# Kernel tuning notes

Hardware: AMD Instinct MI355X
Metric: run time of the kernel (lower is better)

The kernel has to match this reference:

```python
import jax, jax.numpy as jnp
import numpy as np

N_NODES = 100000
N_EDGES = 1600000
D_IN = 128
D_OUT = 128
EPS = 1e-5


def setup_inputs() -> dict:
    key = jax.random.key(0)
    k1, k2, k3, k4, k5 = jax.random.split(key, 5)
    x = jax.random.normal(k1, (N_NODES, D_IN), dtype=jnp.float32)
    row = jax.random.randint(k2, (N_EDGES,), 0, N_NODES, dtype=jnp.int64)
    col = jax.random.randint(k3, (N_EDGES,), 0, N_NODES, dtype=jnp.int64)
    adj_vals = jax.random.uniform(k4, (N_EDGES,), dtype=jnp.float32)
    # Xavier-uniform init for weight, zeros for bias (as in the torch module)
    limit = float(np.sqrt(6.0 / (D_IN + D_OUT)))
    weight = jax.random.uniform(k5, (D_IN, D_OUT), minval=-limit, maxval=limit, dtype=jnp.float32)
    bias = jnp.zeros((D_OUT,), dtype=jnp.float32)
    return {"x": x, "row": row, "col": col, "adj_vals": adj_vals, "weight": weight, "bias": bias}


def reference(x, row, col, adj_vals, weight, bias):
    # degree = row-sum of sparse adj
    degree = jax.ops.segment_sum(adj_vals, row, num_segments=N_NODES)
    degree = jnp.where(degree == 0, EPS, degree)
    d_inv_sqrt = (degree + EPS) ** -0.5  # [N]
    # edge-wise symmetric normalization: D^-1/2 A D^-1/2
    edge_w = d_inv_sqrt[row] * adj_vals * d_inv_sqrt[col]  # [E]
    # SpMM: gather neighbor features, scale, scatter-add to destination rows
    msgs = edge_w[:, None] * x[col]  # [E, D_IN]
    agg = jax.ops.segment_sum(msgs, row, num_segments=N_NODES)  # [N, D_IN]
    return agg @ weight + bias
```

## Files before the change

kernel.cpp:

```cpp
#include <hip/hip_runtime.h>

#define NN 100000
#define NE 1600000
#define D  128
#define EPS 1e-5f

#define NBKT   782
#define NEB    391
#define EPB_H  4096
#define NSCAN  (NBKT*NEB)
#define GRID2  299
#define CAP    2560
#define SLW    16

#define OFF_HCNT 0x0000000ULL
#define OFF_PART 0x0140000ULL
#define OFF_DINV 0x0150000ULL
#define OFF_RBC  0x0200000ULL
#define OFF_GREC 0x0280000ULL
#define OFF_ECOL 0x0F00000ULL
#define OFF_YB   0x1700000ULL

typedef short short8 __attribute__((ext_vector_type(8)));
typedef float f32x4 __attribute__((ext_vector_type(4)));

static __device__ __forceinline__ unsigned f2bf(float f) {
    unsigned u = __float_as_uint(f);
    return (u + 0x7fffu + ((u >> 16) & 1u)) >> 16;
}

__global__ void k0h(const int* __restrict__ row, unsigned* __restrict__ hcnt) {
    __shared__ unsigned h[NBKT];
    int t = threadIdx.x, b = blockIdx.x;
    for (int i = t; i < NBKT; i += 256) h[i] = 0;
    __syncthreads();
    int ebeg = b * EPB_H;
    for (int i = t; i < EPB_H; i += 256) {
        int e = ebeg + i;
        if (e < NE) atomicAdd(&h[((unsigned)row[e]) >> 7], 1u);
    }
    __syncthreads();
    for (int i = t; i < NBKT; i += 256) hcnt[i * NEB + b] = h[i];
}

__global__ void k2a(const unsigned* __restrict__ hcnt, unsigned* __restrict__ part) {
    __shared__ unsigned s[256];
    int t = threadIdx.x;
    int gi = blockIdx.x * 1024 + t * 4;
    unsigned v = 0;
    #pragma unroll
    for (int j = 0; j < 4; ++j) if (gi + j < NSCAN) v += hcnt[gi + j];
    s[t] = v;
    __syncthreads();
    for (int d = 128; d > 0; d >>= 1) {
        if (t < d) s[t] += s[t + d];
        __syncthreads();
    }
    if (t == 0) part[blockIdx.x] = s[0];
}

__global__ void k2c(unsigned* __restrict__ hcnt, const unsigned* __restrict__ part) {
    __shared__ unsigned s[256];
    __shared__ unsigned bbase;
    int t = threadIdx.x, g = blockIdx.x;

    unsigned v = 0;
    for (int i = t; i < g; i += 256) v += part[i];
    s[t] = v;
    __syncthreads();
    for (int d = 128; d > 0; d >>= 1) {
        if (t < d) s[t] += s[t + d];
        __syncthreads();
    }
    if (t == 0) bbase = s[0];
    __syncthreads();
    unsigned base = bbase;
    __syncthreads();

    int gi = g * 1024 + t * 4;
    unsigned w[4], tot = 0;
    #pragma unroll
    for (int j = 0; j < 4; ++j) {
        w[j] = (gi + j < NSCAN) ? hcnt[gi + j] : 0;
        tot += w[j];
    }
    s[t] = tot;
    __syncthreads();
    for (int d = 1; d < 256; d <<= 1) {
        unsigned u = (t >= d) ? s[t - d] : 0;
        __syncthreads();
        s[t] += u;
        __syncthreads();
    }
    unsigned run = base + s[t] - tot;
    #pragma unroll
    for (int j = 0; j < 4; ++j) {
        if (gi + j < NSCAN) { hcnt[gi + j] = run; run += w[j]; }
    }
}

__launch_bounds__(256)
__global__ void k3(const int* __restrict__ row, const int* __restrict__ col,
                   const float* __restrict__ adj, const unsigned* __restrict__ hcnt,
                   unsigned long long* __restrict__ grec) {
    __shared__ unsigned cur[NBKT];
    int t = threadIdx.x, b = blockIdx.x;
    for (int i = t; i < NBKT; i += 256) cur[i] = hcnt[i * NEB + b];
    __syncthreads();
    int ebeg = b * EPB_H;
    for (int i = t; i < EPB_H; i += 256) {
        int e = ebeg + i;
        if (e >= NE) continue;
        unsigned r = (unsigned)row[e];
        unsigned aq = (unsigned)rintf(adj[e] * 32767.0f);
        unsigned lo = (unsigned)col[e] | (aq << 17);
        unsigned dst = atomicAdd(&cur[r >> 7], 1u);
        grec[dst] = (unsigned long long)lo | ((unsigned long long)(r & 127u) << 32);
    }
}

__launch_bounds__(256, 2)
__global__ void k1g(const float* __restrict__ x, const float* __restrict__ w,
                    const unsigned* __restrict__ hcnt,
                    const unsigned long long* __restrict__ grec,
                    float* __restrict__ dinv_g, unsigned* __restrict__ rbcnt_g,
                    unsigned* __restrict__ ecol_g, unsigned short* __restrict__ yb) {
    __shared__ unsigned short sx[128 * 128];
    __shared__ unsigned short sw[128 * 128];
    __shared__ unsigned sdeg[128], scnt[128], srb[128], scur[128];
    __shared__ float sdv[128];
    unsigned* secol = (unsigned*)sx;
    int tid = threadIdx.x;
    int b = blockIdx.x;
    int base = b * 128;

    if (tid < 128) { sdeg[tid] = 0; scnt[tid] = 0; }
    __syncthreads();
    unsigned beg = hcnt[b * NEB];
    unsigned end = (b == NBKT - 1) ? NE : hcnt[(b + 1) * NEB];
    unsigned n = end - beg;
    for (unsigned p = beg + tid; p < end; p += 256) {
        unsigned long long rec = grec[p];
        unsigned rid = (unsigned)(rec >> 32) & 127u;
        atomicAdd(&sdeg[rid], ((unsigned)rec >> 17) & 0x7FFFu);
        atomicAdd(&scnt[rid], 1u);
    }
    __syncthreads();

    if (tid < 128) {
        float d = (float)sdeg[tid] * (1.0f / 32767.0f);
        d = (d == 0.0f) ? EPS : d;
        float dv = rsqrtf(d + EPS);
        sdv[tid] = dv;
        int r = base + tid;
        if (r < NN) dinv_g[r] = dv;
        srb[tid] = scnt[tid];
    }
    __syncthreads();
    for (int dd = 1; dd < 128; dd <<= 1) {
        unsigned u = (tid >= dd && tid < 128) ? srb[tid - dd] : 0;
        __syncthreads();
        if (tid < 128) srb[tid] += u;
        __syncthreads();
    }
    if (tid < 128) {
        unsigned rb = srb[tid] - scnt[tid];
        srb[tid] = rb;
        scur[tid] = rb;
        rbcnt_g[b * 128 + tid] = (rb << 16) | scnt[tid];
    }
    __syncthreads();

    for (unsigned p = beg + tid; p < end; p += 256) {
        unsigned long long rec = grec[p];
        unsigned rank = atomicAdd(&scur[(unsigned)(rec >> 32) & 127u], 1u);
        if (rank < CAP) secol[rank] = (unsigned)rec;
    }
    __syncthreads();
    unsigned ns = min(n, (unsigned)CAP);
    for (unsigned i = tid; i < ns; i += 256) ecol_g[(size_t)b * CAP + i] = secol[i];
    __syncthreads();

    #pragma unroll
    for (int i = 0; i < 8; ++i) {
        int task = i * 256 + tid;
        int nn = task & 127, ko = task >> 7;
        const float* wp = w + (size_t)(ko * 8) * D + nn;
        uint4 pk;
        pk.x = f2bf(wp[0])     | (f2bf(wp[D])     << 16);
        pk.y = f2bf(wp[2 * D]) | (f2bf(wp[3 * D]) << 16);
        pk.z = f2bf(wp[4 * D]) | (f2bf(wp[5 * D]) << 16);
        pk.w = f2bf(wp[6 * D]) | (f2bf(wp[7 * D]) << 16);
        int idx = (nn * 128 + ko * 8) ^ ((nn & 7) << 3);
        *(uint4*)(&sw[idx]) = pk;
    }
    #pragma unroll
    for (int i = 0; i < 8; ++i) {
        int task = i * 256 + tid;
        int ko = task & 15, r = task >> 4;
        int gr = base + r;
        float4 f0 = make_float4(0.f, 0.f, 0.f, 0.f), f1 = f0;
        if (gr < NN) {
            const float* xp = x + (size_t)gr * D + ko * 8;
            f0 = *(const float4*)xp;
            f1 = *(const float4*)(xp + 4);
        }
        uint4 pk;
        pk.x = f2bf(f0.x) | (f2bf(f0.y) << 16);
        pk.y = f2bf(f0.z) | (f2bf(f0.w) << 16);
        pk.z = f2bf(f1.x) | (f2bf(f1.y) << 16);
        pk.w = f2bf(f1.z) | (f2bf(f1.w) << 16);
        int idx = (r * 128 + ko * 8) ^ ((r & 7) << 3);
        *(uint4*)(&sx[idx]) = pk;
    }
    __syncthreads();

    int wv = tid >> 6, l = tid & 63;
    int lr = l & 15, g = l >> 4;

    f32x4 acc[2][8];
    #pragma unroll
    for (int ti = 0; ti < 2; ++ti)
        #pragma unroll
        for (int tj = 0; tj < 8; ++tj)
            acc[ti][tj] = (f32x4){0.f, 0.f, 0.f, 0.f};

    #pragma unroll
    for (int kc = 0; kc < 4; ++kc) {
        int kb = kc * 32 + g * 8;
        short8 a[2], bb[8];
        #pragma unroll
        for (int ti = 0; ti < 2; ++ti) {
            int r0 = wv * 32 + ti * 16 + lr;
            a[ti] = *(const short8*)(&sx[(r0 * 128 + kb) ^ ((r0 & 7) << 3)]);
        }
        #pragma unroll
        for (int tj = 0; tj < 8; ++tj) {
            int n0 = tj * 16 + lr;
            bb[tj] = *(const short8*)(&sw[(n0 * 128 + kb) ^ ((n0 & 7) << 3)]);
        }
        #pragma unroll
        for (int ti = 0; ti < 2; ++ti)
            #pragma unroll
            for (int tj = 0; tj < 8; ++tj)
                acc[ti][tj] = __builtin_amdgcn_mfma_f32_16x16x32_bf16(
                    a[ti], bb[tj], acc[ti][tj], 0, 0, 0);
    }

    #pragma unroll
    for (int ti = 0; ti < 2; ++ti) {
        #pragma unroll
        for (int reg = 0; reg < 4; ++reg) {
            int lrow = wv * 32 + ti * 16 + g * 4 + reg;
            int gr = base + lrow;
            if (gr < NN) {
                float dv = sdv[lrow];
                #pragma unroll
                for (int tj = 0; tj < 8; ++tj)
                    yb[(size_t)tj * (NN * SLW) + (size_t)gr * SLW + lr] =
                        (unsigned short)f2bf(acc[ti][tj][reg] * dv);
            }
        }
    }
}

__launch_bounds__(512, 4)
__global__ void k4b(const unsigned* __restrict__ rbcnt_g, const unsigned* __restrict__ ecol_g,
                    const float* __restrict__ dinv, const unsigned short* __restrict__ ybs,
                    const float* __restrict__ bias, float* __restrict__ out) {
    __shared__ unsigned ecol[CAP + 8];
    __shared__ unsigned rb_l[128], cnt_l[128];
    __shared__ unsigned nsh;
    int t = threadIdx.x, bid = blockIdx.x;
    int s = bid & 7;
    int q = bid >> 3;
    const unsigned short* ys = ybs + (size_t)s * (NN * SLW);

    if (t < 128) {
        unsigned v = rbcnt_g[q * 128 + t];
        rb_l[t] = v >> 16;
        cnt_l[t] = v & 0xFFFFu;
        if (t == 127) nsh = min((v >> 16) + (v & 0xFFFFu), (unsigned)CAP);
    }
    __syncthreads();
    unsigned n = nsh;
    const unsigned* eg = ecol_g + (size_t)q * CAP;
    for (unsigned i = t; i < n; i += 512) ecol[i] = eg[i];
    __syncthreads();

    int grp = t >> 2, lq = t & 3;
    int r = q * 128 + grp;
    if (r >= NN) return;
    unsigned jb = rb_l[grp];
    unsigned jend = min(jb + cnt_l[grp], (unsigned)CAP);

    float a0 = 0.f, a1 = 0.f, a2 = 0.f, a3 = 0.f;

    for (unsigned j = jb; j < jend; j += 8) {
        unsigned ee[8];
        uint2 yq[8];
        float wv[8];
        int cm[8];
        #pragma unroll
        for (int u = 0; u < 8; ++u) ee[u] = ecol[j + u];
        #pragma unroll
        for (int u = 0; u < 8; ++u) cm[u] = min((int)(ee[u] & 0x1FFFFu), NN - 1);
        #pragma unroll
        for (int u = 0; u < 8; ++u)
            yq[u] = *(const uint2*)(ys + (size_t)cm[u] * SLW + lq * 4);
        #pragma unroll
        for (int u = 0; u < 8; ++u)
            wv[u] = (j + u < jend) ? (float)(ee[u] >> 17) : 0.f;
        #pragma unroll
        for (int u = 0; u < 8; ++u) {
            a0 += wv[u] * __uint_as_float(yq[u].x << 16);
            a1 += wv[u] * __uint_as_float(yq[u].x & 0xffff0000u);
            a2 += wv[u] * __uint_as_float(yq[u].y << 16);
            a3 += wv[u] * __uint_as_float(yq[u].y & 0xffff0000u);
        }
    }

    float scale = dinv[r] * (1.0f / 32767.0f);
    float4 bb = *(const float4*)(bias + s * SLW + lq * 4);
    float4 rr = make_float4(a0 * scale + bb.x, a1 * scale + bb.y,
                            a2 * scale + bb.z, a3 * scale + bb.w);
    *(float4*)(out + (size_t)r * D + s * SLW + lq * 4) = rr;
}

extern "C" void kernel_launch(void* const* d_in, const int* in_sizes, int n_in,
                              void* d_out, int out_size, void* d_ws, size_t ws_size,
                              hipStream_t stream) {
    const float* x    = (const float*)d_in[0];
    const int*   row  = (const int*)d_in[1];
    const int*   col  = (const int*)d_in[2];
    const float* adj  = (const float*)d_in[3];
    const float* wgt  = (const float*)d_in[4];
    const float* bias = (const float*)d_in[5];
    float* out = (float*)d_out;
    char*  ws  = (char*)d_ws;

    unsigned* hcnt  = (unsigned*)(ws + OFF_HCNT);
    unsigned* part  = (unsigned*)(ws + OFF_PART);
    float*    dinv  = (float*)(ws + OFF_DINV);
    unsigned* rbcnt = (unsigned*)(ws + OFF_RBC);
    unsigned long long* grec = (unsigned long long*)(ws + OFF_GREC);
    unsigned* ecolg = (unsigned*)(ws + OFF_ECOL);
    unsigned short* yb = (unsigned short*)(ws + OFF_YB);

    k0h<<<NEB, 256, 0, stream>>>(row, hcnt);
    k2a<<<GRID2, 256, 0, stream>>>(hcnt, part);
    k2c<<<GRID2, 256, 0, stream>>>(hcnt, part);
    k3 <<<NEB, 256, 0, stream>>>(row, col, adj, hcnt, grec);
    k1g<<<NBKT, 256, 0, stream>>>(x, wgt, hcnt, grec, dinv, rbcnt, ecolg, yb);
    k4b<<<NBKT * 8, 512, 0, stream>>>(rbcnt, ecolg, dinv, yb, bias, out);
}
```

Measured before the change: 150.0 us.

## Replace global scan with per-bucket scan into fixed-capacity bucket slots; widen SpMM gathers

```diff
diff --git a/kernel.cpp b/kernel.cpp
--- a/kernel.cpp
+++ b/kernel.cpp
@@ -9,17 +9,16 @@
 #define NEB    391
 #define EPB_H  4096
 #define NSCAN  (NBKT*NEB)
-#define GRID2  299
 #define CAP    2560
 #define SLW    16
 
 #define OFF_HCNT 0x0000000ULL
-#define OFF_PART 0x0140000ULL
+#define OFF_BTOT 0x0140000ULL
 #define OFF_DINV 0x0150000ULL
 #define OFF_RBC  0x0200000ULL
 #define OFF_GREC 0x0280000ULL
-#define OFF_ECOL 0x0F00000ULL
-#define OFF_YB   0x1700000ULL
+#define OFF_ECOL 0x11C6000ULL
+#define OFF_YB   0x1A00000ULL
 
 typedef short short8 __attribute__((ext_vector_type(8)));
 typedef float f32x4 __attribute__((ext_vector_type(4)));
@@ -43,48 +42,14 @@
     for (int i = t; i < NBKT; i += 256) hcnt[i * NEB + b] = h[i];
 }
 
-__global__ void k2a(const unsigned* __restrict__ hcnt, unsigned* __restrict__ part) {
+__global__ void k2s(unsigned* __restrict__ hcnt, unsigned* __restrict__ btot) {
     __shared__ unsigned s[256];
-    int t = threadIdx.x;
-    int gi = blockIdx.x * 1024 + t * 4;
-    unsigned v = 0;
-    #pragma unroll
-    for (int j = 0; j < 4; ++j) if (gi + j < NSCAN) v += hcnt[gi + j];
-    s[t] = v;
-    __syncthreads();
-    for (int d = 128; d > 0; d >>= 1) {
-        if (t < d) s[t] += s[t + d];
-        __syncthreads();
-    }
-    if (t == 0) part[blockIdx.x] = s[0];
-}
-
-__global__ void k2c(unsigned* __restrict__ hcnt, const unsigned* __restrict__ part) {
-    __shared__ unsigned s[256];
-    __shared__ unsigned bbase;
-    int t = threadIdx.x, g = blockIdx.x;
-
-    unsigned v = 0;
-    for (int i = t; i < g; i += 256) v += part[i];
-    s[t] = v;
-    __syncthreads();
-    for (int d = 128; d > 0; d >>= 1) {
-        if (t < d) s[t] += s[t + d];
-        __syncthreads();
-    }
-    if (t == 0) bbase = s[0];
-    __syncthreads();
-    unsigned base = bbase;
-    __syncthreads();
-
-    int gi = g * 1024 + t * 4;
-    unsigned w[4], tot = 0;
-    #pragma unroll
-    for (int j = 0; j < 4; ++j) {
-        w[j] = (gi + j < NSCAN) ? hcnt[gi + j] : 0;
-        tot += w[j];
-    }
-    s[t] = tot;
+    int t = threadIdx.x, b = blockIdx.x;
+    unsigned* hp = hcnt + (size_t)b * NEB;
+    unsigned v0 = (2 * t     < NEB) ? hp[2 * t]     : 0;
+    unsigned v1 = (2 * t + 1 < NEB) ? hp[2 * t + 1] : 0;
+    unsigned sum = v0 + v1;
+    s[t] = sum;
     __syncthreads();
     for (int d = 1; d < 256; d <<= 1) {
         unsigned u = (t >= d) ? s[t - d] : 0;
@@ -92,11 +57,10 @@
         s[t] += u;
         __syncthreads();
     }
-    unsigned run = base + s[t] - tot;
-    #pragma unroll
-    for (int j = 0; j < 4; ++j) {
-        if (gi + j < NSCAN) { hcnt[gi + j] = run; run += w[j]; }
-    }
+    unsigned base = s[t] - sum;
+    if (2 * t     < NEB) hp[2 * t]     = base;
+    if (2 * t + 1 < NEB) hp[2 * t + 1] = base + v0;
+    if (t == 255) btot[b] = s[255];
 }
 
 __launch_bounds__(256)
@@ -105,23 +69,26 @@
                    unsigned long long* __restrict__ grec) {
     __shared__ unsigned cur[NBKT];
     int t = threadIdx.x, b = blockIdx.x;
-    for (int i = t; i < NBKT; i += 256) cur[i] = hcnt[i * NEB + b];
+    for (int i = t; i < NBKT; i += 256)
+        cur[i] = (unsigned)i * CAP + hcnt[i * NEB + b];
     __syncthreads();
     int ebeg = b * EPB_H;
     for (int i = t; i < EPB_H; i += 256) {
         int e = ebeg + i;
         if (e >= NE) continue;
         unsigned r = (unsigned)row[e];
+        unsigned bkt = r >> 7;
         unsigned aq = (unsigned)rintf(adj[e] * 32767.0f);
         unsigned lo = (unsigned)col[e] | (aq << 17);
-        unsigned dst = atomicAdd(&cur[r >> 7], 1u);
-        grec[dst] = (unsigned long long)lo | ((unsigned long long)(r & 127u) << 32);
+        unsigned dst = atomicAdd(&cur[bkt], 1u);
+        if (dst < (bkt + 1) * (unsigned)CAP)
+            grec[dst] = (unsigned long long)lo | ((unsigned long long)(r & 127u) << 32);
     }
 }
 
 __launch_bounds__(256, 2)
 __global__ void k1g(const float* __restrict__ x, const float* __restrict__ w,
-                    const unsigned* __restrict__ hcnt,
+                    const unsigned* __restrict__ btot,
                     const unsigned long long* __restrict__ grec,
                     float* __restrict__ dinv_g, unsigned* __restrict__ rbcnt_g,
                     unsigned* __restrict__ ecol_g, unsigned short* __restrict__ yb) {
@@ -136,9 +103,9 @@
 
     if (tid < 128) { sdeg[tid] = 0; scnt[tid] = 0; }
     __syncthreads();
-    unsigned beg = hcnt[b * NEB];
-    unsigned end = (b == NBKT - 1) ? NE : hcnt[(b + 1) * NEB];
-    unsigned n = end - beg;
+    unsigned beg = (unsigned)b * CAP;
+    unsigned n = min(btot[b], (unsigned)CAP);
+    unsigned end = beg + n;
     for (unsigned p = beg + tid; p < end; p += 256) {
         unsigned long long rec = grec[p];
         unsigned rid = (unsigned)(rec >> 32) & 127u;
@@ -177,8 +144,7 @@
         if (rank < CAP) secol[rank] = (unsigned)rec;
     }
     __syncthreads();
-    unsigned ns = min(n, (unsigned)CAP);
-    for (unsigned i = tid; i < ns; i += 256) ecol_g[(size_t)b * CAP + i] = secol[i];
+    for (unsigned i = tid; i < n; i += 256) ecol_g[(size_t)b * CAP + i] = secol[i];
     __syncthreads();
 
     #pragma unroll
@@ -257,14 +223,14 @@
                 float dv = sdv[lrow];
                 #pragma unroll
                 for (int tj = 0; tj < 8; ++tj)
-                    yb[(size_t)tj * (NN * SLW) + (size_t)gr * SLW + lr] =
+                    yb[(size_t)tj * ((size_t)NN * SLW) + (size_t)gr * SLW + lr] =
                         (unsigned short)f2bf(acc[ti][tj][reg] * dv);
             }
         }
     }
 }
 
-__launch_bounds__(512, 4)
+__launch_bounds__(256, 4)
 __global__ void k4b(const unsigned* __restrict__ rbcnt_g, const unsigned* __restrict__ ecol_g,
                     const float* __restrict__ dinv, const unsigned short* __restrict__ ybs,
                     const float* __restrict__ bias, float* __restrict__ out) {
@@ -274,7 +240,7 @@
     int t = threadIdx.x, bid = blockIdx.x;
     int s = bid & 7;
     int q = bid >> 3;
-    const unsigned short* ys = ybs + (size_t)s * (NN * SLW);
+    const unsigned short* ys = ybs + (size_t)s * ((size_t)NN * SLW);
 
     if (t < 128) {
         unsigned v = rbcnt_g[q * 128 + t];
@@ -285,29 +251,32 @@
     __syncthreads();
     unsigned n = nsh;
     const unsigned* eg = ecol_g + (size_t)q * CAP;
-    for (unsigned i = t; i < n; i += 512) ecol[i] = eg[i];
-    __syncthreads();
-
-    int grp = t >> 2, lq = t & 3;
+    for (unsigned i = t; i < n; i += 256) ecol[i] = eg[i];
+    __syncthreads();
+
+    int grp = t >> 1, lq = t & 1;
     int r = q * 128 + grp;
     if (r >= NN) return;
     unsigned jb = rb_l[grp];
     unsigned jend = min(jb + cnt_l[grp], (unsigned)CAP);
 
     float a0 = 0.f, a1 = 0.f, a2 = 0.f, a3 = 0.f;
+    float a4 = 0.f, a5 = 0.f, a6 = 0.f, a7 = 0.f;
 
     for (unsigned j = jb; j < jend; j += 8) {
         unsigned ee[8];
-        uint2 yq[8];
+        uint4 yq[8];
         float wv[8];
         int cm[8];
+        unsigned c0 = ecol[j] & 0x1FFFFu;
         #pragma unroll
         for (int u = 0; u < 8; ++u) ee[u] = ecol[j + u];
         #pragma unroll
-        for (int u = 0; u < 8; ++u) cm[u] = min((int)(ee[u] & 0x1FFFFu), NN - 1);
-        #pragma unroll
         for (int u = 0; u < 8; ++u)
-            yq[u] = *(const uint2*)(ys + (size_t)cm[u] * SLW + lq * 4);
+            cm[u] = (j + u < jend) ? (int)(ee[u] & 0x1FFFFu) : (int)c0;
+        #pragma unroll
+        for (int u = 0; u < 8; ++u)
+            yq[u] = *(const uint4*)(ys + (size_t)cm[u] * SLW + lq * 8);
         #pragma unroll
         for (int u = 0; u < 8; ++u)
             wv[u] = (j + u < jend) ? (float)(ee[u] >> 17) : 0.f;
@@ -317,14 +286,21 @@
             a1 += wv[u] * __uint_as_float(yq[u].x & 0xffff0000u);
             a2 += wv[u] * __uint_as_float(yq[u].y << 16);
             a3 += wv[u] * __uint_as_float(yq[u].y & 0xffff0000u);
+            a4 += wv[u] * __uint_as_float(yq[u].z << 16);
+            a5 += wv[u] * __uint_as_float(yq[u].z & 0xffff0000u);
+            a6 += wv[u] * __uint_as_float(yq[u].w << 16);
+            a7 += wv[u] * __uint_as_float(yq[u].w & 0xffff0000u);
         }
     }
 
     float scale = dinv[r] * (1.0f / 32767.0f);
-    float4 bb = *(const float4*)(bias + s * SLW + lq * 4);
-    float4 rr = make_float4(a0 * scale + bb.x, a1 * scale + bb.y,
-                            a2 * scale + bb.z, a3 * scale + bb.w);
-    *(float4*)(out + (size_t)r * D + s * SLW + lq * 4) = rr;
+    const float4* bp = (const float4*)(bias + s * SLW + lq * 8);
+    float4* op = (float4*)(out + (size_t)r * D + s * SLW + lq * 8);
+    float4 b0 = bp[0], b1 = bp[1];
+    op[0] = make_float4(a0 * scale + b0.x, a1 * scale + b0.y,
+                        a2 * scale + b0.z, a3 * scale + b0.w);
+    op[1] = make_float4(a4 * scale + b1.x, a5 * scale + b1.y,
+                        a6 * scale + b1.z, a7 * scale + b1.w);
 }
 
 extern "C" void kernel_launch(void* const* d_in, const int* in_sizes, int n_in,
@@ -340,7 +316,7 @@
     char*  ws  = (char*)d_ws;
 
     unsigned* hcnt  = (unsigned*)(ws + OFF_HCNT);
-    unsigned* part  = (unsigned*)(ws + OFF_PART);
+    unsigned* btot  = (unsigned*)(ws + OFF_BTOT);
     float*    dinv  = (float*)(ws + OFF_DINV);
     unsigned* rbcnt = (unsigned*)(ws + OFF_RBC);
     unsigned long long* grec = (unsigned long long*)(ws + OFF_GREC);
@@ -348,9 +324,8 @@
     unsigned short* yb = (unsigned short*)(ws + OFF_YB);
 
     k0h<<<NEB, 256, 0, stream>>>(row, hcnt);
-    k2a<<<GRID2, 256, 0, stream>>>(hcnt, part);
-    k2c<<<GRID2, 256, 0, stream>>>(hcnt, part);
+    k2s<<<NBKT, 256, 0, stream>>>(hcnt, btot);
     k3 <<<NEB, 256, 0, stream>>>(row, col, adj, hcnt, grec);
-    k1g<<<NBKT, 256, 0, stream>>>(x, wgt, hcnt, grec, dinv, rbcnt, ecolg, yb);
-    k4b<<<NBKT * 8, 512, 0, stream>>>(rbcnt, ecolg, dinv, yb, bias, out);
-}
+    k1g<<<NBKT, 256, 0, stream>>>(x, wgt, btot, grec, dinv, rbcnt, ecolg, yb);
+    k4b<<<NBKT * 8, 256, 0, stream>>>(rbcnt, ecolg, dinv, yb, bias, out);
+}
```

Measured after the change: 148.1 us. No clear change (-1.3%).
